# Kernel tuning notes

Hardware: AMD Instinct MI355X
Metric: run time of the kernel (lower is better)

The kernel has to match this reference:

```python
import jax, jax.numpy as jnp
import numpy as np

M = 7            # window_size
NUM_HEADS = 12
C = 384
D_HEAD = C // NUM_HEADS
SCALE = D_HEAD ** (-0.5)


def _relative_position_index(m):
    coords = np.stack(np.meshgrid(np.arange(m), np.arange(m), indexing='ij')).reshape(2, -1)
    rel = coords[:, :, None] - coords[:, None, :]          # [2, m^2, m^2]
    rel = rel.transpose(1, 2, 0).astype(np.int64)          # [m^2, m^2, 2]
    rel[..., 0] += m - 1
    rel[..., 1] += m - 1
    rel[..., 0] *= 2 * m - 1
    return jnp.asarray(rel.sum(-1))                         # [m^2, m^2]

REL_INDEX = _relative_position_index(M)


def setup_inputs() -> dict:
    key = jax.random.key(0)
    ks = jax.random.split(key, 7)
    B_, N = 4096, M * M
    x = jax.random.normal(ks[0], (B_, N, C), dtype=jnp.float32)
    mask = jax.random.normal(ks[1], (64, N, N), dtype=jnp.float32)
    bias_table = 0.02 * jax.random.normal(ks[2], ((2 * M - 1) * (2 * M - 1), NUM_HEADS), dtype=jnp.float32)
    qkv_w = 0.02 * jax.random.normal(ks[3], (3 * C, C), dtype=jnp.float32)
    qkv_b = jnp.zeros((3 * C,), dtype=jnp.float32)
    proj_w = 0.02 * jax.random.normal(ks[4], (C, C), dtype=jnp.float32)
    proj_b = jnp.zeros((C,), dtype=jnp.float32)
    return {"x": x, "mask": mask, "bias_table": bias_table,
            "qkv_w": qkv_w, "qkv_b": qkv_b, "proj_w": proj_w, "proj_b": proj_b}


def reference(x, mask, bias_table, qkv_w, qkv_b, proj_w, proj_b):
    B_, N, _ = x.shape
    H, d = NUM_HEADS, D_HEAD
    qkv = x @ qkv_w.T + qkv_b                              # [B_, N, 3C]
    qkv = qkv.reshape(B_, N, 3, H, d)
    q = qkv[:, :, 0].transpose(0, 2, 1, 3)                 # [B_, H, N, d]
    k = qkv[:, :, 1].transpose(0, 2, 1, 3)
    v = qkv[:, :, 2].transpose(0, 2, 1, 3)
    attn = jnp.einsum('bhnd,bhmd->bhnm', q, k) * SCALE     # [B_, H, N, N]
    bias = bias_table[REL_INDEX.reshape(-1)].reshape(N, N, H).transpose(2, 0, 1)
    attn = attn + bias[None]
    nW = mask.shape[0]
    attn = attn.reshape(B_ // nW, nW, H, N, N) + mask[None, :, None]
    attn = attn.reshape(B_, H, N, N)
    attn = jax.nn.softmax(attn, axis=-1)
    out = jnp.einsum('bhnm,bhmd->bhnd', attn, v)           # [B_, H, N, d]
    out = out.transpose(0, 2, 1, 3).reshape(B_, N, C)
    return out @ proj_w.T + proj_b
```

## Files before the change

kernel.cpp:

```cpp
#include <hip/hip_runtime.h>
#include <stdint.h>

typedef __attribute__((ext_vector_type(8))) short bf16x8;
typedef __attribute__((ext_vector_type(4))) short bf16x4;
typedef __attribute__((ext_vector_type(4))) float f32x4;
typedef __attribute__((ext_vector_type(2))) unsigned int u32x2;

#define NSCALE 0.17677669529663687f

static __device__ __forceinline__ float bf2f(unsigned short h) {
  union { unsigned int u; float f; } c; c.u = ((unsigned int)h) << 16; return c.f;
}
static __device__ __forceinline__ unsigned short f2bf(float f) {
  union { float f; unsigned int u; } c; c.f = f;
  unsigned int u = c.u;
  u = (u + 0x7FFFu + ((u >> 16) & 1u)) >> 16;
  return (unsigned short)u;
}
static __device__ __forceinline__ unsigned int packbf2(float a, float b) {
  return (unsigned int)f2bf(a) | ((unsigned int)f2bf(b) << 16);
}

#define W_QKVW  0
#define W_PROJW 442368
#define W_BIASE 589824
#define W_ELEMS 619240
#define W_BYTES (W_ELEMS * 2)

__global__ void cvt_w_kernel(const float* __restrict__ qkv_w,
                             const float* __restrict__ proj_w,
                             unsigned short* __restrict__ ws) {
  const int i = blockIdx.x * 256 + threadIdx.x;
  const int stride = gridDim.x * 256;
  for (int e = i; e < 442368; e += stride)
    ws[W_QKVW + e] = f2bf(qkv_w[e] * (e < 147456 ? NSCALE : 1.f));
  for (int e = i; e < 147456; e += stride)
    ws[W_PROJW + e] = f2bf(proj_w[e]);
}

__global__ void biase_kernel(const float* __restrict__ bias_t,
                             unsigned short* __restrict__ ws) {
  const int h = blockIdx.x;
  unsigned short* dst = ws + W_BIASE + h * 2450;
  for (int e = threadIdx.x; e < 2401; e += 256) {
    const int q = e / 49, k = e - q * 49;
    const int i1 = q / 7, j1 = q - i1 * 7;
    const int i2 = k / 7, j2 = k - i2 * 7;
    const int ridx = (i1 - i2 + 6) * 13 + (j1 - j2 + 6);
    dst[q * 50 + k] = f2bf(bias_t[ridx * 12 + h]);
  }
}

#define XS_O  0
#define U_O   19208
#define QS_O  (U_O)
#define KS_O  (U_O + 3920)
#define VT_O  (U_O + 7840)
#define MSP_O (U_O + 12448)
#define LDS_EL (U_O + 12448 + 2458)
#define LDS_BYTES2 (LDS_EL * 2)

__global__ void __launch_bounds__(256)
__attribute__((amdgpu_waves_per_eu(1, 8)))
winattn8(const float* __restrict__ x,
         const float* __restrict__ mask,
         const float* __restrict__ qkv_b,
         const float* __restrict__ proj_b,
         const unsigned short* __restrict__ ws,
         float* __restrict__ out)
{
  extern __shared__ unsigned short sm[];
  unsigned short* Xs  = sm + XS_O;
  unsigned short* Qs  = sm + QS_O;
  unsigned short* Ks  = sm + KS_O;
  unsigned short* Vt  = sm + VT_O;
  unsigned short* Msp = sm + MSP_O;
  unsigned short* Os  = sm + XS_O;

  const unsigned short* wsQW = ws + W_QKVW;
  const unsigned short* wsPW = ws + W_PROJW;
  const unsigned short* wsBE = ws + W_BIASE;

  const int b = blockIdx.x;
  const int tid = threadIdx.x;
  const int w = tid >> 6, lane = tid & 63, l15 = lane & 15, lg = lane >> 4;

  const float* xw = x + b * 18816;
  for (int e = tid; e < 4704; e += 256) {
    const int f = e << 2;
    const int r = f / 384;
    const int c = f - r * 384;
    f32x4 v = *(const f32x4*)(xw + f);
    u32x2 pk; pk[0] = packbf2(v[0], v[1]); pk[1] = packbf2(v[2], v[3]);
    *(u32x2*)(Xs + r * 392 + c) = pk;
  }
  {
    const float* mw = mask + (b & 63) * 2401;
    for (int e = tid; e < 2401; e += 256) {
      const int q = e / 49, k = e - q * 49;
      Msp[q * 50 + k] = f2bf(mw[e]);
    }
  }
  __syncthreads();

  const int q  = w * 16 + l15;
  const int qc = q > 48 ? 48 : q;

  unsigned int opk[6][2][2][2];

  for (int g = 0; g < 6; ++g) {
#pragma unroll
    for (int i = 0; i < 3; ++i) {
      const int nt = 3 * w + i;
      const int s = nt >> 2, sub = nt & 3, hh = sub >> 1, half = sub & 1;
      const int dd = (half << 4) + l15;
      const int o = s * 384 + (2 * g + hh) * 32 + dd;
      const unsigned short* wr = wsQW + o * 384 + lg * 8;
      f32x4 acc[4];
#pragma unroll
      for (int mi = 0; mi < 4; ++mi) acc[mi] = (f32x4){0.f, 0.f, 0.f, 0.f};
#pragma unroll
      for (int c2 = 0; c2 < 2; ++c2) {
        bf16x8 Bf[6];
#pragma unroll
        for (int cc = 0; cc < 6; ++cc) Bf[cc] = *(const bf16x8*)(wr + (c2 * 6 + cc) * 32);
#pragma unroll
        for (int mi = 0; mi < 4; ++mi) {
          const int ar = mi * 16 + l15;
          const unsigned short* ap = Xs + (ar > 48 ? 48 : ar) * 392 + lg * 8;
#pragma unroll
          for (int cc = 0; cc < 6; ++cc) {
            bf16x8 Af = *(const bf16x8*)(ap + (c2 * 6 + cc) * 32);
            acc[mi] = __builtin_amdgcn_mfma_f32_16x16x32_bf16(Af, Bf[cc], acc[mi], 0, 0, 0);
          }
        }
      }
      const float bias = qkv_b[o] * (s == 0 ? NSCALE : 1.f);
      if (s < 2) {
        unsigned short* T = (s == 0 ? Qs : Ks) + hh * 1960 + dd;
#pragma unroll
        for (int mi = 0; mi < 4; ++mi)
#pragma unroll
          for (int j = 0; j < 4; ++j) {
            const int row = mi * 16 + lg * 4 + j;
            if (row < 49) T[row * 40] = f2bf(acc[mi][j] + bias);
          }
      } else {
#pragma unroll
        for (int mi = 0; mi < 4; ++mi) {
          bf16x4 pk;
#pragma unroll
          for (int j = 0; j < 4; ++j) pk[j] = (short)f2bf(acc[mi][j] + bias);
          *(bf16x4*)(Vt + hh * 2304 + dd * 72 + mi * 16 + lg * 4) = pk;
        }
      }
    }
    __syncthreads();

#pragma unroll
    for (int hh = 0; hh < 2; ++hh) {
      const int head = 2 * g + hh;
      bf16x8 Qf = *(const bf16x8*)(Qs + hh * 1960 + qc * 40 + lg * 8);
      f32x4 S[4];
#pragma unroll
      for (int mt = 0; mt < 4; ++mt) {
        const int kr = mt * 16 + l15;
        bf16x8 Kf = *(const bf16x8*)(Ks + hh * 1960 + (kr > 48 ? 48 : kr) * 40 + lg * 8);
        f32x4 z = {0.f, 0.f, 0.f, 0.f};
        S[mt] = __builtin_amdgcn_mfma_f32_16x16x32_bf16(Kf, Qf, z, 0, 0, 0);
      }
      const unsigned short* be = wsBE + head * 2450 + qc * 50;
      const unsigned short* ms = Msp + qc * 50;
      float p[16];
      float vmax = -3e30f;
#pragma unroll
      for (int mt = 0; mt < 4; ++mt) {
        const int kc0 = mt * 16 + lg * 4;
        const int ko = kc0 > 48 ? 48 : kc0;
        const unsigned int b01 = *(const unsigned int*)(be + ko);
        const unsigned int b23 = *(const unsigned int*)(be + ko + 2);
        const unsigned int m01 = *(const unsigned int*)(ms + ko);
        const unsigned int m23 = *(const unsigned int*)(ms + ko + 2);
        float ad0 = bf2f((unsigned short)(b01 & 0xffff)) + bf2f((unsigned short)(m01 & 0xffff));
        float ad1 = bf2f((unsigned short)(b01 >> 16))    + bf2f((unsigned short)(m01 >> 16));
        float ad2 = bf2f((unsigned short)(b23 & 0xffff)) + bf2f((unsigned short)(m23 & 0xffff));
        float ad3 = bf2f((unsigned short)(b23 >> 16))    + bf2f((unsigned short)(m23 >> 16));
        float v0 = S[mt][0] + ad0, v1 = S[mt][1] + ad1;
        float v2 = S[mt][2] + ad2, v3 = S[mt][3] + ad3;
        if (kc0 + 0 >= 49) v0 = -3e30f;
        if (kc0 + 1 >= 49) v1 = -3e30f;
        if (kc0 + 2 >= 49) v2 = -3e30f;
        if (kc0 + 3 >= 49) v3 = -3e30f;
        p[mt * 4 + 0] = v0; p[mt * 4 + 1] = v1;
        p[mt * 4 + 2] = v2; p[mt * 4 + 3] = v3;
        vmax = fmaxf(fmaxf(fmaxf(v0, v1), fmaxf(v2, v3)), vmax);
      }
      vmax = fmaxf(vmax, __shfl_xor(vmax, 16, 64));
      vmax = fmaxf(vmax, __shfl_xor(vmax, 32, 64));
      float ssum = 0.f;
#pragma unroll
      for (int i = 0; i < 16; ++i) { p[i] = __expf(p[i] - vmax); ssum += p[i]; }
      ssum += __shfl_xor(ssum, 16, 64);
      ssum += __shfl_xor(ssum, 32, 64);
      const float rs = 1.f / ssum;
      unsigned int plo[4], phi[4];
#pragma unroll
      for (int mt = 0; mt < 4; ++mt) {
        plo[mt] = packbf2(p[mt * 4 + 0], p[mt * 4 + 1]);
        phi[mt] = packbf2(p[mt * 4 + 2], p[mt * 4 + 3]);
      }
      union { bf16x8 v; unsigned int u[4]; } PB[2];
      const int src0 = l15 + ((lg & 1) << 5);
      const int src1 = src0 + 16;
      const int sel = lg >> 1;
#pragma unroll
      for (int ks = 0; ks < 2; ++ks) {
        const int a0 = __shfl((int)plo[2 * ks], src0, 64), a1 = __shfl((int)plo[2 * ks + 1], src0, 64);
        const int b0 = __shfl((int)phi[2 * ks], src0, 64), b1 = __shfl((int)phi[2 * ks + 1], src0, 64);
        const int c0 = __shfl((int)plo[2 * ks], src1, 64), c1 = __shfl((int)plo[2 * ks + 1], src1, 64);
        const int d0 = __shfl((int)phi[2 * ks], src1, 64), d1 = __shfl((int)phi[2 * ks + 1], src1, 64);
        PB[ks].u[0] = (unsigned)(sel ? a1 : a0);
        PB[ks].u[1] = (unsigned)(sel ? b1 : b0);
        PB[ks].u[2] = (unsigned)(sel ? c1 : c0);
        PB[ks].u[3] = (unsigned)(sel ? d1 : d0);
      }
#pragma unroll
      for (int dt = 0; dt < 2; ++dt) {
        f32x4 a = {0.f, 0.f, 0.f, 0.f};
#pragma unroll
        for (int ks = 0; ks < 2; ++ks) {
          bf16x8 Vf = *(const bf16x8*)(Vt + hh * 2304 + (dt * 16 + l15) * 72 + ks * 32 + lg * 8);
          a = __builtin_amdgcn_mfma_f32_16x16x32_bf16(Vf, PB[ks].v, a, 0, 0, 0);
        }
        const unsigned int lo = packbf2(a[0] * rs, a[1] * rs);
        const unsigned int hi = packbf2(a[2] * rs, a[3] * rs);
        switch (g) {
          case 0: opk[0][hh][dt][0] = lo; opk[0][hh][dt][1] = hi; break;
          case 1: opk[1][hh][dt][0] = lo; opk[1][hh][dt][1] = hi; break;
          case 2: opk[2][hh][dt][0] = lo; opk[2][hh][dt][1] = hi; break;
          case 3: opk[3][hh][dt][0] = lo; opk[3][hh][dt][1] = hi; break;
          case 4: opk[4][hh][dt][0] = lo; opk[4][hh][dt][1] = hi; break;
          default: opk[5][hh][dt][0] = lo; opk[5][hh][dt][1] = hi; break;
        }
      }
    }
    __syncthreads();
  }

  if (q < 49) {
#pragma unroll
    for (int gg = 0; gg < 6; ++gg)
#pragma unroll
      for (int hh = 0; hh < 2; ++hh)
#pragma unroll
        for (int dt = 0; dt < 2; ++dt) {
          u32x2 pk; pk[0] = opk[gg][hh][dt][0]; pk[1] = opk[gg][hh][dt][1];
          *(u32x2*)(Os + q * 392 + (2 * gg + hh) * 32 + dt * 16 + lg * 4) = pk;
        }
  }
  __syncthreads();

#pragma unroll
  for (int ntl = 0; ntl < 6; ++ntl) {
    const int co = (6 * w + ntl) * 16 + l15;
    const unsigned short* wr = wsPW + co * 384 + lg * 8;
    const float pb = proj_b[co];
    f32x4 acc[4];
#pragma unroll
    for (int mt = 0; mt < 4; ++mt) acc[mt] = (f32x4){0.f, 0.f, 0.f, 0.f};
#pragma unroll
    for (int c2 = 0; c2 < 2; ++c2) {
      bf16x8 Bf[6];
#pragma unroll
      for (int cc = 0; cc < 6; ++cc) Bf[cc] = *(const bf16x8*)(wr + (c2 * 6 + cc) * 32);
#pragma unroll
      for (int mt = 0; mt < 4; ++mt) {
        const int ar = mt * 16 + l15;
        const unsigned short* ap = Os + (ar > 48 ? 48 : ar) * 392 + lg * 8;
#pragma unroll
        for (int cc = 0; cc < 6; ++cc) {
          bf16x8 Af = *(const bf16x8*)(ap + (c2 * 6 + cc) * 32);
          acc[mt] = __builtin_amdgcn_mfma_f32_16x16x32_bf16(Af, Bf[cc], acc[mt], 0, 0, 0);
        }
      }
    }
#pragma unroll
    for (int mt = 0; mt < 4; ++mt)
#pragma unroll
      for (int j = 0; j < 4; ++j) {
        const int row = mt * 16 + lg * 4 + j;
        if (row < 49) out[b * 18816 + row * 384 + co] = acc[mt][j] + pb;
      }
  }
}

#define FXS 0
#define FQS (FXS + 64*392)
#define FKS (FQS + 2*64*40)
#define FVT (FKS + 2*64*40)
#define FPS (FVT + 2*32*72)
#define FOS (FPS + 2*64*72)
#define FMS (FOS + 64*392)
#define FBS (FMS + 2408)
#define FLDS_EL (FBS + 2028)
#define FLDS_BYTES (FLDS_EL * 2)

static __device__ __forceinline__ bf16x8 cvt8(const float* p) {
  f32x4 a = *(const f32x4*)p;
  f32x4 b = *(const f32x4*)(p + 4);
  bf16x8 r;
  r[0]=(short)f2bf(a[0]); r[1]=(short)f2bf(a[1]); r[2]=(short)f2bf(a[2]); r[3]=(short)f2bf(a[3]);
  r[4]=(short)f2bf(b[0]); r[5]=(short)f2bf(b[1]); r[6]=(short)f2bf(b[2]); r[7]=(short)f2bf(b[3]);
  return r;
}

__global__ __launch_bounds__(512, 2)
void winattn_fb(const float* __restrict__ x, const float* __restrict__ mask,
                const float* __restrict__ bias_t, const float* __restrict__ qkv_w,
                const float* __restrict__ qkv_b, const float* __restrict__ proj_w,
                const float* __restrict__ proj_b, float* __restrict__ out)
{
  extern __shared__ unsigned short sm[];
  unsigned short* Xs = sm + FXS; unsigned short* Qs = sm + FQS;
  unsigned short* Ks = sm + FKS; unsigned short* Vt = sm + FVT;
  unsigned short* Ps = sm + FPS; unsigned short* Os = sm + FOS;
  unsigned short* Ms = sm + FMS; unsigned short* Bs = sm + FBS;
  const int b = blockIdx.x, tid = threadIdx.x;
  const int w = tid >> 6, lane = tid & 63, l15 = lane & 15, lg = lane >> 4;
  const float* xw = x + b * 18816;
  for (int e = tid; e < 4704; e += 512) {
    const int f = e << 2; const int r = f / 384; const int c = f - r * 384;
    f32x4 v = *(const f32x4*)(xw + f);
    unsigned short* dst = Xs + r * 392 + c;
    dst[0]=f2bf(v[0]); dst[1]=f2bf(v[1]); dst[2]=f2bf(v[2]); dst[3]=f2bf(v[3]);
  }
  { bf16x8 z = {0,0,0,0,0,0,0,0};
    for (int e = tid; e < 735; e += 512) *(bf16x8*)(Xs + 19208 + (e << 3)) = z; }
  { const float* mw = mask + (b & 63) * 2401;
    for (int e = tid; e < 2401; e += 512) Ms[e] = f2bf(mw[e]);
    for (int e = tid; e < 2028; e += 512) Bs[e] = f2bf(bias_t[e]); }
  __syncthreads();
  for (int g = 0; g < 6; ++g) {
    int t = 6 * w; const int tEnd = t + 6;
    while (t < tEnd) {
      const int nt = t >> 2; const int hh = nt / 6; const int ntl = nt - hh * 6;
      const int s = ntl >> 1; const int dd = ((nt & 1) << 4) + l15;
      const int o = s * 384 + (2 * g + hh) * 32 + dd;
      bf16x8 Bf[12];
      const float* wp = qkv_w + o * 384 + lg * 8;
#pragma unroll
      for (int kk = 0; kk < 12; ++kk) Bf[kk] = cvt8(wp + kk * 32);
      const float biasc = qkv_b[o];
      for (; t < tEnd && (t >> 2) == nt; ++t) {
        const int mt = t & 3;
        f32x4 acc = {0.f,0.f,0.f,0.f};
        const unsigned short* ap = Xs + (mt * 16 + l15) * 392 + lg * 8;
#pragma unroll
        for (int kk = 0; kk < 12; ++kk) {
          bf16x8 Af = *(const bf16x8*)(ap + kk * 32);
          acc = __builtin_amdgcn_mfma_f32_16x16x32_bf16(Af, Bf[kk], acc, 0,0,0);
        }
#pragma unroll
        for (int j = 0; j < 4; ++j) {
          const int row = mt * 16 + lg * 4 + j;
          const unsigned short hv = f2bf(acc[j] + biasc);
          if (s == 0) Qs[hh * 2560 + row * 40 + dd] = hv;
          else if (s == 1) Ks[hh * 2560 + row * 40 + dd] = hv;
          else Vt[hh * 2304 + dd * 72 + row] = hv;
        }
      }
    }
    __syncthreads();
    {
      const int hh = w >> 2; const int mt = w & 3; const int head = 2 * g + hh;
      bf16x8 Aq = *(const bf16x8*)(Qs + hh * 2560 + (mt * 16 + l15) * 40 + lg * 8);
      f32x4 accs[4];
#pragma unroll
      for (int nt = 0; nt < 4; ++nt) {
        bf16x8 Bk = *(const bf16x8*)(Ks + hh * 2560 + (nt * 16 + l15) * 40 + lg * 8);
        f32x4 z = {0.f,0.f,0.f,0.f};
        accs[nt] = __builtin_amdgcn_mfma_f32_16x16x32_bf16(Aq, Bk, z, 0,0,0);
      }
#pragma unroll
      for (int j = 0; j < 4; ++j) {
        const int row = mt * 16 + lg * 4 + j;
        float sv[4]; float vmax = -3e30f;
#pragma unroll
        for (int nt = 0; nt < 4; ++nt) {
          const int col = nt * 16 + l15;
          float v = accs[nt][j] * NSCALE;
          if (col < 49) { if (row < 49) {
              const int i1 = row / 7, j1 = row - i1 * 7;
              const int i2 = col / 7, j2 = col - i2 * 7;
              const int ridx = (i1 - i2 + 6) * 13 + (j1 - j2 + 6);
              v += bf2f(Ms[row * 49 + col]) + bf2f(Bs[ridx * 12 + head]); } }
          else v = -3e30f;
          sv[nt] = v; vmax = fmaxf(vmax, v);
        }
#pragma unroll
        for (int mm = 1; mm < 16; mm <<= 1) vmax = fmaxf(vmax, __shfl_xor(vmax, mm, 64));
        float ssum = 0.f;
#pragma unroll
        for (int nt = 0; nt < 4; ++nt) { sv[nt] = __expf(sv[nt] - vmax); ssum += sv[nt]; }
#pragma unroll
        for (int mm = 1; mm < 16; mm <<= 1) ssum += __shfl_xor(ssum, mm, 64);
        const float rs = 1.f / ssum;
#pragma unroll
        for (int nt = 0; nt < 4; ++nt)
          Ps[hh * 4608 + row * 72 + nt * 16 + l15] = f2bf(sv[nt] * rs);
      }
    }
    __syncthreads();
    {
      const int hh = w >> 2; const int mt = w & 3; const int head = 2 * g + hh;
#pragma unroll
      for (int nt = 0; nt < 2; ++nt) {
        f32x4 acc = {0.f,0.f,0.f,0.f};
#pragma unroll
        for (int kk = 0; kk < 2; ++kk) {
          bf16x8 Ap = *(const bf16x8*)(Ps + hh * 4608 + (mt * 16 + l15) * 72 + kk * 32 + lg * 8);
          bf16x8 Bv = *(const bf16x8*)(Vt + hh * 2304 + (nt * 16 + l15) * 72 + kk * 32 + lg * 8);
          acc = __builtin_amdgcn_mfma_f32_16x16x32_bf16(Ap, Bv, acc, 0,0,0);
        }
#pragma unroll
        for (int j = 0; j < 4; ++j)
          Os[(mt * 16 + lg * 4 + j) * 392 + head * 32 + nt * 16 + l15] = f2bf(acc[j]);
      }
    }
    __syncthreads();
  }
  for (int nt = 3 * w; nt < 3 * w + 3; ++nt) {
    const int co = nt * 16 + l15;
    bf16x8 Bf[12];
    const float* wp = proj_w + co * 384 + lg * 8;
#pragma unroll
    for (int kk = 0; kk < 12; ++kk) Bf[kk] = cvt8(wp + kk * 32);
    const float pb = proj_b[co];
#pragma unroll
    for (int mt = 0; mt < 4; ++mt) {
      f32x4 acc = {0.f,0.f,0.f,0.f};
      const unsigned short* ap = Os + (mt * 16 + l15) * 392 + lg * 8;
#pragma unroll
      for (int kk = 0; kk < 12; ++kk) {
        bf16x8 Af = *(const bf16x8*)(ap + kk * 32);
        acc = __builtin_amdgcn_mfma_f32_16x16x32_bf16(Af, Bf[kk], acc, 0,0,0);
      }
#pragma unroll
      for (int j = 0; j < 4; ++j) {
        const int row = mt * 16 + lg * 4 + j;
        if (row < 49) out[b * 18816 + row * 384 + co] = acc[j] + pb;
      }
    }
  }
}

extern "C" void kernel_launch(void* const* d_in, const int* in_sizes, int n_in,
                              void* d_out, int out_size, void* d_ws, size_t ws_size,
                              hipStream_t stream) {
  const float* x      = (const float*)d_in[0];
  const float* mask   = (const float*)d_in[1];
  const float* bias_t = (const float*)d_in[2];
  const float* qkv_w  = (const float*)d_in[3];
  const float* qkv_b  = (const float*)d_in[4];
  const float* proj_w = (const float*)d_in[5];
  const float* proj_b = (const float*)d_in[6];
  float* out = (float*)d_out;

  if (ws_size >= (size_t)W_BYTES) {
    unsigned short* ws = (unsigned short*)d_ws;
    cvt_w_kernel<<<dim3(1024), dim3(256), 0, stream>>>(qkv_w, proj_w, ws);
    biase_kernel<<<dim3(12), dim3(256), 0, stream>>>(bias_t, ws);
    (void)hipFuncSetAttribute((const void*)winattn8,
                              hipFuncAttributeMaxDynamicSharedMemorySize, LDS_BYTES2);
    winattn8<<<dim3(4096), dim3(256), LDS_BYTES2, stream>>>(
        x, mask, qkv_b, proj_b, ws, out);
  } else {
    (void)hipFuncSetAttribute((const void*)winattn_fb,
                              hipFuncAttributeMaxDynamicSharedMemorySize, FLDS_BYTES);
    winattn_fb<<<dim3(4096), dim3(512), FLDS_BYTES, stream>>>(
        x, mask, bias_t, qkv_w, qkv_b, proj_w, proj_b, out);
  }
}
```

Before: 801.7 us.

## Switch QKV and output projection GEMMs to 32x32x16 MFMA tiles

Replaces the 16x16x32 MFMA tiling of the QKV and projection GEMMs with 32x32x16 MFMA. Each wave now owns a 32-row half of the 49-token window and a set of 32-column output tiles. The aim is fewer LDS A-fragment reloads per MFMA and fewer padded rows (64 vs 49 handled as two 32-row tiles). In exchange the accumulators are larger (f32x16), which may raise register pressure, and the epilogue store pattern changes to a scattered row layout. The B fragments are now streamed from global memory each k-step rather than batched.

```diff
diff --git a/kernel.cpp b/kernel.cpp
--- a/kernel.cpp
+++ b/kernel.cpp
@@ -4,9 +4,11 @@
 typedef __attribute__((ext_vector_type(8))) short bf16x8;
 typedef __attribute__((ext_vector_type(4))) short bf16x4;
 typedef __attribute__((ext_vector_type(4))) float f32x4;
+typedef __attribute__((ext_vector_type(16))) float f32x16;
 typedef __attribute__((ext_vector_type(2))) unsigned int u32x2;
 
 #define NSCALE 0.17677669529663687f
+#define Z16 ((f32x16){0.f,0.f,0.f,0.f,0.f,0.f,0.f,0.f,0.f,0.f,0.f,0.f,0.f,0.f,0.f,0.f})
 
 static __device__ __forceinline__ float bf2f(unsigned short h) {
   union { unsigned int u; float f; } c; c.u = ((unsigned int)h) << 16; return c.f;
@@ -60,9 +62,33 @@
 #define LDS_EL (U_O + 12448 + 2458)
 #define LDS_BYTES2 (LDS_EL * 2)
 
+static __device__ __forceinline__ void store_qkv_tile(
+    unsigned short* Qs, unsigned short* Ks, unsigned short* Vt,
+    int t, int m0, int l31, int lhalf, float bias, const f32x16& a)
+{
+  const int s = t >> 1, hh = t & 1;
+  if (s < 2) {
+    unsigned short* T = (s == 0 ? Qs : Ks) + hh * 1960 + l31;
+#pragma unroll
+    for (int r = 0; r < 16; ++r) {
+      const int row = m0 + (r & 3) + 8 * (r >> 2) + 4 * lhalf;
+      if (row < 49) T[row * 40] = f2bf(a[r] + bias);
+    }
+  } else {
+    unsigned short* Vp = Vt + hh * 2304 + l31 * 72 + m0;
+#pragma unroll
+    for (int rq = 0; rq < 4; ++rq) {
+      bf16x4 pk;
+#pragma unroll
+      for (int j = 0; j < 4; ++j) pk[j] = (short)f2bf(a[rq * 4 + j] + bias);
+      *(bf16x4*)(Vp + 8 * rq + 4 * lhalf) = pk;
+    }
+  }
+}
+
 __global__ void __launch_bounds__(256)
 __attribute__((amdgpu_waves_per_eu(1, 8)))
-winattn8(const float* __restrict__ x,
+winattn9(const float* __restrict__ x,
          const float* __restrict__ mask,
          const float* __restrict__ qkv_b,
          const float* __restrict__ proj_b,
@@ -84,6 +110,7 @@
   const int b = blockIdx.x;
   const int tid = threadIdx.x;
   const int w = tid >> 6, lane = tid & 63, l15 = lane & 15, lg = lane >> 4;
+  const int l31 = lane & 31, lhalf = lane >> 5;
 
   const float* xw = x + b * 18816;
   for (int e = tid; e < 4704; e += 256) {
@@ -103,63 +130,59 @@
   }
   __syncthreads();
 
+  const int m0 = (w & 1) * 32;
+  const int nset = w >> 1;
+  const int arow = (m0 + l31) > 48 ? 48 : (m0 + l31);
+  const unsigned short* apA = Xs + arow * 392 + lhalf * 8;
+
   const int q  = w * 16 + l15;
   const int qc = q > 48 ? 48 : q;
 
   unsigned int opk[6][2][2][2];
 
   for (int g = 0; g < 6; ++g) {
-#pragma unroll
-    for (int i = 0; i < 3; ++i) {
-      const int nt = 3 * w + i;
-      const int s = nt >> 2, sub = nt & 3, hh = sub >> 1, half = sub & 1;
-      const int dd = (half << 4) + l15;
-      const int o = s * 384 + (2 * g + hh) * 32 + dd;
-      const unsigned short* wr = wsQW + o * 384 + lg * 8;
-      f32x4 acc[4];
-#pragma unroll
-      for (int mi = 0; mi < 4; ++mi) acc[mi] = (f32x4){0.f, 0.f, 0.f, 0.f};
-#pragma unroll
-      for (int c2 = 0; c2 < 2; ++c2) {
-        bf16x8 Bf[6];
-#pragma unroll
-        for (int cc = 0; cc < 6; ++cc) Bf[cc] = *(const bf16x8*)(wr + (c2 * 6 + cc) * 32);
-#pragma unroll
-        for (int mi = 0; mi < 4; ++mi) {
-          const int ar = mi * 16 + l15;
-          const unsigned short* ap = Xs + (ar > 48 ? 48 : ar) * 392 + lg * 8;
-#pragma unroll
-          for (int cc = 0; cc < 6; ++cc) {
-            bf16x8 Af = *(const bf16x8*)(ap + (c2 * 6 + cc) * 32);
-            acc[mi] = __builtin_amdgcn_mfma_f32_16x16x32_bf16(Af, Bf[cc], acc[mi], 0, 0, 0);
-          }
-        }
-      }
-      const float bias = qkv_b[o] * (s == 0 ? NSCALE : 1.f);
-      if (s < 2) {
-        unsigned short* T = (s == 0 ? Qs : Ks) + hh * 1960 + dd;
-#pragma unroll
-        for (int mi = 0; mi < 4; ++mi)
-#pragma unroll
-          for (int j = 0; j < 4; ++j) {
-            const int row = mi * 16 + lg * 4 + j;
-            if (row < 49) T[row * 40] = f2bf(acc[mi][j] + bias);
-          }
-      } else {
-#pragma unroll
-        for (int mi = 0; mi < 4; ++mi) {
-          bf16x4 pk;
-#pragma unroll
-          for (int j = 0; j < 4; ++j) pk[j] = (short)f2bf(acc[mi][j] + bias);
-          *(bf16x4*)(Vt + hh * 2304 + dd * 72 + mi * 16 + lg * 4) = pk;
-        }
+    const int hb = 2 * g;
+    {
+      const int t0 = 3 * nset;
+      {
+        const int oA = (t0 >> 1) * 384 + (hb + (t0 & 1)) * 32 + l31;
+        const int oB = ((t0 + 1) >> 1) * 384 + (hb + ((t0 + 1) & 1)) * 32 + l31;
+        const unsigned short* bp0 = wsQW + oA * 384 + lhalf * 8;
+        const unsigned short* bp1 = wsQW + oB * 384 + lhalf * 8;
+        f32x16 a0 = Z16, a1 = Z16;
+#pragma unroll 4
+        for (int kc = 0; kc < 24; ++kc) {
+          bf16x8 Af = *(const bf16x8*)(apA + kc * 16);
+          bf16x8 B0 = *(const bf16x8*)(bp0 + kc * 16);
+          bf16x8 B1 = *(const bf16x8*)(bp1 + kc * 16);
+          a0 = __builtin_amdgcn_mfma_f32_32x32x16_bf16(Af, B0, a0, 0, 0, 0);
+          a1 = __builtin_amdgcn_mfma_f32_32x32x16_bf16(Af, B1, a1, 0, 0, 0);
+        }
+        const float bias0 = qkv_b[oA] * ((t0 >> 1) == 0 ? NSCALE : 1.f);
+        const float bias1 = qkv_b[oB] * (((t0 + 1) >> 1) == 0 ? NSCALE : 1.f);
+        store_qkv_tile(Qs, Ks, Vt, t0,     m0, l31, lhalf, bias0, a0);
+        store_qkv_tile(Qs, Ks, Vt, t0 + 1, m0, l31, lhalf, bias1, a1);
+      }
+      {
+        const int t2 = t0 + 2;
+        const int oC = (t2 >> 1) * 384 + (hb + (t2 & 1)) * 32 + l31;
+        const unsigned short* bp2 = wsQW + oC * 384 + lhalf * 8;
+        f32x16 a2 = Z16;
+#pragma unroll 4
+        for (int kc = 0; kc < 24; ++kc) {
+          bf16x8 Af = *(const bf16x8*)(apA + kc * 16);
+          bf16x8 B2 = *(const bf16x8*)(bp2 + kc * 16);
+          a2 = __builtin_amdgcn_mfma_f32_32x32x16_bf16(Af, B2, a2, 0, 0, 0);
+        }
+        const float bias2 = qkv_b[oC] * ((t2 >> 1) == 0 ? NSCALE : 1.f);
+        store_qkv_tile(Qs, Ks, Vt, t2, m0, l31, lhalf, bias2, a2);
       }
     }
     __syncthreads();
 
 #pragma unroll
     for (int hh = 0; hh < 2; ++hh) {
-      const int head = 2 * g + hh;
+      const int head = hb + hh;
       bf16x8 Qf = *(const bf16x8*)(Qs + hh * 1960 + qc * 40 + lg * 8);
       f32x4 S[4];
 #pragma unroll
@@ -260,37 +283,34 @@
   }
   __syncthreads();
 
-#pragma unroll
-  for (int ntl = 0; ntl < 6; ++ntl) {
-    const int co = (6 * w + ntl) * 16 + l15;
-    const unsigned short* wr = wsPW + co * 384 + lg * 8;
-    const float pb = proj_b[co];
-    f32x4 acc[4];
-#pragma unroll
-    for (int mt = 0; mt < 4; ++mt) acc[mt] = (f32x4){0.f, 0.f, 0.f, 0.f};
-#pragma unroll
-    for (int c2 = 0; c2 < 2; ++c2) {
-      bf16x8 Bf[6];
-#pragma unroll
-      for (int cc = 0; cc < 6; ++cc) Bf[cc] = *(const bf16x8*)(wr + (c2 * 6 + cc) * 32);
-#pragma unroll
-      for (int mt = 0; mt < 4; ++mt) {
-        const int ar = mt * 16 + l15;
-        const unsigned short* ap = Os + (ar > 48 ? 48 : ar) * 392 + lg * 8;
-#pragma unroll
-        for (int cc = 0; cc < 6; ++cc) {
-          bf16x8 Af = *(const bf16x8*)(ap + (c2 * 6 + cc) * 32);
-          acc[mt] = __builtin_amdgcn_mfma_f32_16x16x32_bf16(Af, Bf[cc], acc[mt], 0, 0, 0);
-        }
-      }
-    }
-#pragma unroll
-    for (int mt = 0; mt < 4; ++mt)
-#pragma unroll
-      for (int j = 0; j < 4; ++j) {
-        const int row = mt * 16 + lg * 4 + j;
-        if (row < 49) out[b * 18816 + row * 384 + co] = acc[mt][j] + pb;
-      }
+  {
+    const unsigned short* apO = Os + arow * 392 + lhalf * 8;
+    float* ob = out + (size_t)b * 18816;
+#pragma unroll
+    for (int pp = 0; pp < 3; ++pp) {
+      const int n0 = (nset * 6 + 2 * pp) * 32;
+      const unsigned short* bp0 = wsPW + (n0 + l31) * 384 + lhalf * 8;
+      const unsigned short* bp1 = wsPW + (n0 + 32 + l31) * 384 + lhalf * 8;
+      f32x16 a0 = Z16, a1 = Z16;
+#pragma unroll 4
+      for (int kc = 0; kc < 24; ++kc) {
+        bf16x8 Af = *(const bf16x8*)(apO + kc * 16);
+        bf16x8 B0 = *(const bf16x8*)(bp0 + kc * 16);
+        bf16x8 B1 = *(const bf16x8*)(bp1 + kc * 16);
+        a0 = __builtin_amdgcn_mfma_f32_32x32x16_bf16(Af, B0, a0, 0, 0, 0);
+        a1 = __builtin_amdgcn_mfma_f32_32x32x16_bf16(Af, B1, a1, 0, 0, 0);
+      }
+      const float pb0 = proj_b[n0 + l31];
+      const float pb1 = proj_b[n0 + 32 + l31];
+#pragma unroll
+      for (int r = 0; r < 16; ++r) {
+        const int row = m0 + (r & 3) + 8 * (r >> 2) + 4 * lhalf;
+        if (row < 49) {
+          ob[row * 384 + n0 + l31]      = a0[r] + pb0;
+          ob[row * 384 + n0 + 32 + l31] = a1[r] + pb1;
+        }
+      }
+    }
   }
 }
 
@@ -470,9 +490,9 @@
     unsigned short* ws = (unsigned short*)d_ws;
     cvt_w_kernel<<<dim3(1024), dim3(256), 0, stream>>>(qkv_w, proj_w, ws);
     biase_kernel<<<dim3(12), dim3(256), 0, stream>>>(bias_t, ws);
-    (void)hipFuncSetAttribute((const void*)winattn8,
+    (void)hipFuncSetAttribute((const void*)winattn9,
                               hipFuncAttributeMaxDynamicSharedMemorySize, LDS_BYTES2);
-    winattn8<<<dim3(4096), dim3(256), LDS_BYTES2, stream>>>(
+    winattn9<<<dim3(4096), dim3(256), LDS_BYTES2, stream>>>(
         x, mask, qkv_b, proj_b, ws, out);
   } else {
     (void)hipFuncSetAttribute((const void*)winattn_fb,
```

Result: slower. 1.262 ms (+57.5%).

## Partition GEMMs by row tiles per wave with register-resident A fragments

Applied to the files above, without the earlier changes.

The QKV and projection GEMMs are repartitioned so each wave owns one 16-row tile and loops over all output column tiles, keeping its 12 A fragments of X (and later O) in registers. This removes repeated LDS reads of A, but every wave now streams the full weight matrix from global/L2 rather than a third or a quarter of it. The attention output is written to LDS directly each group, dropping the 96-register opk buffer and its switch-based register indexing, along with one barrier.

```diff
diff --git a/kernel.cpp b/kernel.cpp
--- a/kernel.cpp
+++ b/kernel.cpp
@@ -62,12 +62,12 @@
 
 __global__ void __launch_bounds__(256)
 __attribute__((amdgpu_waves_per_eu(1, 8)))
-winattn8(const float* __restrict__ x,
-         const float* __restrict__ mask,
-         const float* __restrict__ qkv_b,
-         const float* __restrict__ proj_b,
-         const unsigned short* __restrict__ ws,
-         float* __restrict__ out)
+winattn10(const float* __restrict__ x,
+          const float* __restrict__ mask,
+          const float* __restrict__ qkv_b,
+          const float* __restrict__ proj_b,
+          const unsigned short* __restrict__ ws,
+          float* __restrict__ out)
 {
   extern __shared__ unsigned short sm[];
   unsigned short* Xs  = sm + XS_O;
@@ -103,63 +103,69 @@
   }
   __syncthreads();
 
+  const int arow = (w * 16 + l15) > 48 ? 48 : (w * 16 + l15);
+  bf16x8 Af[12];
+#pragma unroll
+  for (int kk = 0; kk < 12; ++kk)
+    Af[kk] = *(const bf16x8*)(Xs + arow * 392 + kk * 32 + lg * 8);
+
   const int q  = w * 16 + l15;
   const int qc = q > 48 ? 48 : q;
 
-  unsigned int opk[6][2][2][2];
-
   for (int g = 0; g < 6; ++g) {
-#pragma unroll
-    for (int i = 0; i < 3; ++i) {
-      const int nt = 3 * w + i;
-      const int s = nt >> 2, sub = nt & 3, hh = sub >> 1, half = sub & 1;
-      const int dd = (half << 4) + l15;
-      const int o = s * 384 + (2 * g + hh) * 32 + dd;
-      const unsigned short* wr = wsQW + o * 384 + lg * 8;
-      f32x4 acc[4];
-#pragma unroll
-      for (int mi = 0; mi < 4; ++mi) acc[mi] = (f32x4){0.f, 0.f, 0.f, 0.f};
-#pragma unroll
-      for (int c2 = 0; c2 < 2; ++c2) {
-        bf16x8 Bf[6];
-#pragma unroll
-        for (int cc = 0; cc < 6; ++cc) Bf[cc] = *(const bf16x8*)(wr + (c2 * 6 + cc) * 32);
-#pragma unroll
-        for (int mi = 0; mi < 4; ++mi) {
-          const int ar = mi * 16 + l15;
-          const unsigned short* ap = Xs + (ar > 48 ? 48 : ar) * 392 + lg * 8;
-#pragma unroll
-          for (int cc = 0; cc < 6; ++cc) {
-            bf16x8 Af = *(const bf16x8*)(ap + (c2 * 6 + cc) * 32);
-            acc[mi] = __builtin_amdgcn_mfma_f32_16x16x32_bf16(Af, Bf[cc], acc[mi], 0, 0, 0);
-          }
-        }
-      }
-      const float bias = qkv_b[o] * (s == 0 ? NSCALE : 1.f);
-      if (s < 2) {
-        unsigned short* T = (s == 0 ? Qs : Ks) + hh * 1960 + dd;
-#pragma unroll
-        for (int mi = 0; mi < 4; ++mi)
-#pragma unroll
-          for (int j = 0; j < 4; ++j) {
-            const int row = mi * 16 + lg * 4 + j;
-            if (row < 49) T[row * 40] = f2bf(acc[mi][j] + bias);
-          }
+    const int hb = 2 * g;
+#pragma unroll
+    for (int np = 0; np < 6; ++np) {
+      const int nt0 = 2 * np, nt1 = 2 * np + 1;
+      const int s0 = nt0 >> 2, sub0 = nt0 & 3, hh0 = sub0 >> 1, hf0 = sub0 & 1;
+      const int s1 = nt1 >> 2, sub1 = nt1 & 3, hh1 = sub1 >> 1, hf1 = sub1 & 1;
+      const int o0 = s0 * 384 + (hb + hh0) * 32 + hf0 * 16 + l15;
+      const int o1 = s1 * 384 + (hb + hh1) * 32 + hf1 * 16 + l15;
+      const unsigned short* bp0 = wsQW + o0 * 384 + lg * 8;
+      const unsigned short* bp1 = wsQW + o1 * 384 + lg * 8;
+      f32x4 a0 = {0.f, 0.f, 0.f, 0.f};
+      f32x4 a1 = {0.f, 0.f, 0.f, 0.f};
+#pragma unroll
+      for (int kk = 0; kk < 12; ++kk) {
+        bf16x8 B0 = *(const bf16x8*)(bp0 + kk * 32);
+        bf16x8 B1 = *(const bf16x8*)(bp1 + kk * 32);
+        a0 = __builtin_amdgcn_mfma_f32_16x16x32_bf16(Af[kk], B0, a0, 0, 0, 0);
+        a1 = __builtin_amdgcn_mfma_f32_16x16x32_bf16(Af[kk], B1, a1, 0, 0, 0);
+      }
+      const float bias0 = qkv_b[o0] * (s0 == 0 ? NSCALE : 1.f);
+      const float bias1 = qkv_b[o1] * (s1 == 0 ? NSCALE : 1.f);
+      if (s0 < 2) {
+        unsigned short* T = (s0 == 0 ? Qs : Ks) + hh0 * 1960 + hf0 * 16 + l15;
+#pragma unroll
+        for (int j = 0; j < 4; ++j) {
+          const int row = w * 16 + lg * 4 + j;
+          if (row < 49) T[row * 40] = f2bf(a0[j] + bias0);
+        }
       } else {
-#pragma unroll
-        for (int mi = 0; mi < 4; ++mi) {
-          bf16x4 pk;
-#pragma unroll
-          for (int j = 0; j < 4; ++j) pk[j] = (short)f2bf(acc[mi][j] + bias);
-          *(bf16x4*)(Vt + hh * 2304 + dd * 72 + mi * 16 + lg * 4) = pk;
-        }
+        bf16x4 pk;
+#pragma unroll
+        for (int j = 0; j < 4; ++j) pk[j] = (short)f2bf(a0[j] + bias0);
+        *(bf16x4*)(Vt + hh0 * 2304 + (hf0 * 16 + l15) * 72 + w * 16 + lg * 4) = pk;
+      }
+      if (s1 < 2) {
+        unsigned short* T = (s1 == 0 ? Qs : Ks) + hh1 * 1960 + hf1 * 16 + l15;
+#pragma unroll
+        for (int j = 0; j < 4; ++j) {
+          const int row = w * 16 + lg * 4 + j;
+          if (row < 49) T[row * 40] = f2bf(a1[j] + bias1);
+        }
+      } else {
+        bf16x4 pk;
+#pragma unroll
+        for (int j = 0; j < 4; ++j) pk[j] = (short)f2bf(a1[j] + bias1);
+        *(bf16x4*)(Vt + hh1 * 2304 + (hf1 * 16 + l15) * 72 + w * 16 + lg * 4) = pk;
       }
     }
     __syncthreads();
 
 #pragma unroll
     for (int hh = 0; hh < 2; ++hh) {
-      const int head = 2 * g + hh;
+      const int head = hb + hh;
       bf16x8 Qf = *(const bf16x8*)(Qs + hh * 1960 + qc * 40 + lg * 8);
       f32x4 S[4];
 #pragma unroll
@@ -232,65 +238,49 @@
           bf16x8 Vf = *(const bf16x8*)(Vt + hh * 2304 + (dt * 16 + l15) * 72 + ks * 32 + lg * 8);
           a = __builtin_amdgcn_mfma_f32_16x16x32_bf16(Vf, PB[ks].v, a, 0, 0, 0);
         }
-        const unsigned int lo = packbf2(a[0] * rs, a[1] * rs);
-        const unsigned int hi = packbf2(a[2] * rs, a[3] * rs);
-        switch (g) {
-          case 0: opk[0][hh][dt][0] = lo; opk[0][hh][dt][1] = hi; break;
-          case 1: opk[1][hh][dt][0] = lo; opk[1][hh][dt][1] = hi; break;
-          case 2: opk[2][hh][dt][0] = lo; opk[2][hh][dt][1] = hi; break;
-          case 3: opk[3][hh][dt][0] = lo; opk[3][hh][dt][1] = hi; break;
-          case 4: opk[4][hh][dt][0] = lo; opk[4][hh][dt][1] = hi; break;
-          default: opk[5][hh][dt][0] = lo; opk[5][hh][dt][1] = hi; break;
+        if (q < 49) {
+          u32x2 pk;
+          pk[0] = packbf2(a[0] * rs, a[1] * rs);
+          pk[1] = packbf2(a[2] * rs, a[3] * rs);
+          *(u32x2*)(Os + q * 392 + head * 32 + dt * 16 + lg * 4) = pk;
         }
       }
     }
     __syncthreads();
   }
 
-  if (q < 49) {
-#pragma unroll
-    for (int gg = 0; gg < 6; ++gg)
-#pragma unroll
-      for (int hh = 0; hh < 2; ++hh)
-#pragma unroll
-        for (int dt = 0; dt < 2; ++dt) {
-          u32x2 pk; pk[0] = opk[gg][hh][dt][0]; pk[1] = opk[gg][hh][dt][1];
-          *(u32x2*)(Os + q * 392 + (2 * gg + hh) * 32 + dt * 16 + lg * 4) = pk;
-        }
-  }
-  __syncthreads();
-
-#pragma unroll
-  for (int ntl = 0; ntl < 6; ++ntl) {
-    const int co = (6 * w + ntl) * 16 + l15;
-    const unsigned short* wr = wsPW + co * 384 + lg * 8;
-    const float pb = proj_b[co];
-    f32x4 acc[4];
-#pragma unroll
-    for (int mt = 0; mt < 4; ++mt) acc[mt] = (f32x4){0.f, 0.f, 0.f, 0.f};
-#pragma unroll
-    for (int c2 = 0; c2 < 2; ++c2) {
-      bf16x8 Bf[6];
-#pragma unroll
-      for (int cc = 0; cc < 6; ++cc) Bf[cc] = *(const bf16x8*)(wr + (c2 * 6 + cc) * 32);
-#pragma unroll
-      for (int mt = 0; mt < 4; ++mt) {
-        const int ar = mt * 16 + l15;
-        const unsigned short* ap = Os + (ar > 48 ? 48 : ar) * 392 + lg * 8;
-#pragma unroll
-        for (int cc = 0; cc < 6; ++cc) {
-          bf16x8 Af = *(const bf16x8*)(ap + (c2 * 6 + cc) * 32);
-          acc[mt] = __builtin_amdgcn_mfma_f32_16x16x32_bf16(Af, Bf[cc], acc[mt], 0, 0, 0);
-        }
-      }
-    }
-#pragma unroll
-    for (int mt = 0; mt < 4; ++mt)
+  {
+    bf16x8 Ao[12];
+#pragma unroll
+    for (int kk = 0; kk < 12; ++kk)
+      Ao[kk] = *(const bf16x8*)(Os + arow * 392 + kk * 32 + lg * 8);
+    float* ob = out + (size_t)b * 18816;
+#pragma unroll
+    for (int np = 0; np < 12; ++np) {
+      const int co0 = (2 * np) * 16 + l15;
+      const int co1 = co0 + 16;
+      const unsigned short* bp0 = wsPW + co0 * 384 + lg * 8;
+      const unsigned short* bp1 = wsPW + co1 * 384 + lg * 8;
+      f32x4 a0 = {0.f, 0.f, 0.f, 0.f};
+      f32x4 a1 = {0.f, 0.f, 0.f, 0.f};
+#pragma unroll
+      for (int kk = 0; kk < 12; ++kk) {
+        bf16x8 B0 = *(const bf16x8*)(bp0 + kk * 32);
+        bf16x8 B1 = *(const bf16x8*)(bp1 + kk * 32);
+        a0 = __builtin_amdgcn_mfma_f32_16x16x32_bf16(Ao[kk], B0, a0, 0, 0, 0);
+        a1 = __builtin_amdgcn_mfma_f32_16x16x32_bf16(Ao[kk], B1, a1, 0, 0, 0);
+      }
+      const float pb0 = proj_b[co0];
+      const float pb1 = proj_b[co1];
 #pragma unroll
       for (int j = 0; j < 4; ++j) {
-        const int row = mt * 16 + lg * 4 + j;
-        if (row < 49) out[b * 18816 + row * 384 + co] = acc[mt][j] + pb;
-      }
+        const int row = w * 16 + lg * 4 + j;
+        if (row < 49) {
+          ob[row * 384 + co0] = a0[j] + pb0;
+          ob[row * 384 + co1] = a1[j] + pb1;
+        }
+      }
+    }
   }
 }
 
@@ -470,9 +460,9 @@
     unsigned short* ws = (unsigned short*)d_ws;
     cvt_w_kernel<<<dim3(1024), dim3(256), 0, stream>>>(qkv_w, proj_w, ws);
     biase_kernel<<<dim3(12), dim3(256), 0, stream>>>(bias_t, ws);
-    (void)hipFuncSetAttribute((const void*)winattn8,
+    (void)hipFuncSetAttribute((const void*)winattn10,
                               hipFuncAttributeMaxDynamicSharedMemorySize, LDS_BYTES2);
-    winattn8<<<dim3(4096), dim3(256), LDS_BYTES2, stream>>>(
+    winattn10<<<dim3(4096), dim3(256), LDS_BYTES2, stream>>>(
         x, mask, qkv_b, proj_b, ws, out);
   } else {
     (void)hipFuncSetAttribute((const void*)winattn_fb,
```

After: 2.292 ms. 2.86x slower.

## Reorder QKV and projection GEMM loops to reuse A fragments across output tiles

Applied to the files above, without the earlier changes.

Both the QKV and output-projection MFMA loops now iterate over K chunks outermost. Each step loads four A fragments from LDS once and reuses them across three output tiles, where before the A tile was reloaded for every output tile. This cuts LDS read traffic by about three times but holds twelve accumulators at once, raising register pressure. The waves-per-EU hint is changed from (1,8) to (2,4) to give the compiler room for the extra registers.

```diff
diff --git a/kernel.cpp b/kernel.cpp
--- a/kernel.cpp
+++ b/kernel.cpp
@@ -61,13 +61,13 @@
 #define LDS_BYTES2 (LDS_EL * 2)
 
 __global__ void __launch_bounds__(256)
-__attribute__((amdgpu_waves_per_eu(1, 8)))
-winattn8(const float* __restrict__ x,
-         const float* __restrict__ mask,
-         const float* __restrict__ qkv_b,
-         const float* __restrict__ proj_b,
-         const unsigned short* __restrict__ ws,
-         float* __restrict__ out)
+__attribute__((amdgpu_waves_per_eu(2, 4)))
+winattn11(const float* __restrict__ x,
+          const float* __restrict__ mask,
+          const float* __restrict__ qkv_b,
+          const float* __restrict__ proj_b,
+          const unsigned short* __restrict__ ws,
+          float* __restrict__ out)
 {
   extern __shared__ unsigned short sm[];
   unsigned short* Xs  = sm + XS_O;
@@ -109,57 +109,70 @@
   unsigned int opk[6][2][2][2];
 
   for (int g = 0; g < 6; ++g) {
-#pragma unroll
-    for (int i = 0; i < 3; ++i) {
-      const int nt = 3 * w + i;
-      const int s = nt >> 2, sub = nt & 3, hh = sub >> 1, half = sub & 1;
-      const int dd = (half << 4) + l15;
-      const int o = s * 384 + (2 * g + hh) * 32 + dd;
-      const unsigned short* wr = wsQW + o * 384 + lg * 8;
-      f32x4 acc[4];
-#pragma unroll
-      for (int mi = 0; mi < 4; ++mi) acc[mi] = (f32x4){0.f, 0.f, 0.f, 0.f};
-#pragma unroll
-      for (int c2 = 0; c2 < 2; ++c2) {
-        bf16x8 Bf[6];
-#pragma unroll
-        for (int cc = 0; cc < 6; ++cc) Bf[cc] = *(const bf16x8*)(wr + (c2 * 6 + cc) * 32);
+    const int hb = 2 * g;
+    {
+      const int ntb = 3 * w;
+      const unsigned short* bp[3];
+      float bias[3];
+#pragma unroll
+      for (int i = 0; i < 3; ++i) {
+        const int nt = ntb + i;
+        const int s = nt >> 2, sub = nt & 3, hh = sub >> 1, hf = sub & 1;
+        const int o = s * 384 + (hb + hh) * 32 + hf * 16 + l15;
+        bp[i] = wsQW + o * 384 + lg * 8;
+        bias[i] = qkv_b[o] * (s == 0 ? NSCALE : 1.f);
+      }
+      f32x4 acc[3][4];
+#pragma unroll
+      for (int i = 0; i < 3; ++i)
+#pragma unroll
+        for (int mi = 0; mi < 4; ++mi) acc[i][mi] = (f32x4){0.f, 0.f, 0.f, 0.f};
+#pragma unroll
+      for (int kk = 0; kk < 12; ++kk) {
+        bf16x8 A4[4];
 #pragma unroll
         for (int mi = 0; mi < 4; ++mi) {
           const int ar = mi * 16 + l15;
-          const unsigned short* ap = Xs + (ar > 48 ? 48 : ar) * 392 + lg * 8;
-#pragma unroll
-          for (int cc = 0; cc < 6; ++cc) {
-            bf16x8 Af = *(const bf16x8*)(ap + (c2 * 6 + cc) * 32);
-            acc[mi] = __builtin_amdgcn_mfma_f32_16x16x32_bf16(Af, Bf[cc], acc[mi], 0, 0, 0);
+          A4[mi] = *(const bf16x8*)(Xs + (ar > 48 ? 48 : ar) * 392 + kk * 32 + lg * 8);
+        }
+        bf16x8 B3[3];
+#pragma unroll
+        for (int i = 0; i < 3; ++i) B3[i] = *(const bf16x8*)(bp[i] + kk * 32);
+#pragma unroll
+        for (int i = 0; i < 3; ++i)
+#pragma unroll
+          for (int mi = 0; mi < 4; ++mi)
+            acc[i][mi] = __builtin_amdgcn_mfma_f32_16x16x32_bf16(A4[mi], B3[i], acc[i][mi], 0, 0, 0);
+      }
+#pragma unroll
+      for (int i = 0; i < 3; ++i) {
+        const int nt = ntb + i;
+        const int s = nt >> 2, sub = nt & 3, hh = sub >> 1, hf = sub & 1;
+        if (s < 2) {
+          unsigned short* T = (s == 0 ? Qs : Ks) + hh * 1960 + hf * 16 + l15;
+#pragma unroll
+          for (int mi = 0; mi < 4; ++mi)
+#pragma unroll
+            for (int j = 0; j < 4; ++j) {
+              const int row = mi * 16 + lg * 4 + j;
+              if (row < 49) T[row * 40] = f2bf(acc[i][mi][j] + bias[i]);
+            }
+        } else {
+#pragma unroll
+          for (int mi = 0; mi < 4; ++mi) {
+            bf16x4 pk;
+#pragma unroll
+            for (int j = 0; j < 4; ++j) pk[j] = (short)f2bf(acc[i][mi][j] + bias[i]);
+            *(bf16x4*)(Vt + hh * 2304 + (hf * 16 + l15) * 72 + mi * 16 + lg * 4) = pk;
           }
         }
       }
-      const float bias = qkv_b[o] * (s == 0 ? NSCALE : 1.f);
-      if (s < 2) {
-        unsigned short* T = (s == 0 ? Qs : Ks) + hh * 1960 + dd;
-#pragma unroll
-        for (int mi = 0; mi < 4; ++mi)
-#pragma unroll
-          for (int j = 0; j < 4; ++j) {
-            const int row = mi * 16 + lg * 4 + j;
-            if (row < 49) T[row * 40] = f2bf(acc[mi][j] + bias);
-          }
-      } else {
-#pragma unroll
-        for (int mi = 0; mi < 4; ++mi) {
-          bf16x4 pk;
-#pragma unroll
-          for (int j = 0; j < 4; ++j) pk[j] = (short)f2bf(acc[mi][j] + bias);
-          *(bf16x4*)(Vt + hh * 2304 + dd * 72 + mi * 16 + lg * 4) = pk;
-        }
-      }
     }
     __syncthreads();
 
 #pragma unroll
     for (int hh = 0; hh < 2; ++hh) {
-      const int head = 2 * g + hh;
+      const int head = hb + hh;
       bf16x8 Qf = *(const bf16x8*)(Qs + hh * 1960 + qc * 40 + lg * 8);
       f32x4 S[4];
 #pragma unroll
@@ -260,37 +273,51 @@
   }
   __syncthreads();
 
-#pragma unroll
-  for (int ntl = 0; ntl < 6; ++ntl) {
-    const int co = (6 * w + ntl) * 16 + l15;
-    const unsigned short* wr = wsPW + co * 384 + lg * 8;
-    const float pb = proj_b[co];
-    f32x4 acc[4];
-#pragma unroll
-    for (int mt = 0; mt < 4; ++mt) acc[mt] = (f32x4){0.f, 0.f, 0.f, 0.f};
-#pragma unroll
-    for (int c2 = 0; c2 < 2; ++c2) {
-      bf16x8 Bf[6];
-#pragma unroll
-      for (int cc = 0; cc < 6; ++cc) Bf[cc] = *(const bf16x8*)(wr + (c2 * 6 + cc) * 32);
-#pragma unroll
-      for (int mt = 0; mt < 4; ++mt) {
-        const int ar = mt * 16 + l15;
-        const unsigned short* ap = Os + (ar > 48 ? 48 : ar) * 392 + lg * 8;
-#pragma unroll
-        for (int cc = 0; cc < 6; ++cc) {
-          bf16x8 Af = *(const bf16x8*)(ap + (c2 * 6 + cc) * 32);
-          acc[mt] = __builtin_amdgcn_mfma_f32_16x16x32_bf16(Af, Bf[cc], acc[mt], 0, 0, 0);
-        }
-      }
-    }
-#pragma unroll
-    for (int mt = 0; mt < 4; ++mt)
-#pragma unroll
-      for (int j = 0; j < 4; ++j) {
-        const int row = mt * 16 + lg * 4 + j;
-        if (row < 49) out[b * 18816 + row * 384 + co] = acc[mt][j] + pb;
-      }
+  {
+    float* ob = out + (size_t)b * 18816;
+#pragma unroll
+    for (int pp = 0; pp < 2; ++pp) {
+      const unsigned short* bp[3];
+      float pb[3];
+      int co[3];
+#pragma unroll
+      for (int i = 0; i < 3; ++i) {
+        co[i] = (6 * w + 3 * pp + i) * 16 + l15;
+        bp[i] = wsPW + co[i] * 384 + lg * 8;
+        pb[i] = proj_b[co[i]];
+      }
+      f32x4 acc[3][4];
+#pragma unroll
+      for (int i = 0; i < 3; ++i)
+#pragma unroll
+        for (int mi = 0; mi < 4; ++mi) acc[i][mi] = (f32x4){0.f, 0.f, 0.f, 0.f};
+#pragma unroll
+      for (int kk = 0; kk < 12; ++kk) {
+        bf16x8 A4[4];
+#pragma unroll
+        for (int mi = 0; mi < 4; ++mi) {
+          const int ar = mi * 16 + l15;
+          A4[mi] = *(const bf16x8*)(Os + (ar > 48 ? 48 : ar) * 392 + kk * 32 + lg * 8);
+        }
+        bf16x8 B3[3];
+#pragma unroll
+        for (int i = 0; i < 3; ++i) B3[i] = *(const bf16x8*)(bp[i] + kk * 32);
+#pragma unroll
+        for (int i = 0; i < 3; ++i)
+#pragma unroll
+          for (int mi = 0; mi < 4; ++mi)
+            acc[i][mi] = __builtin_amdgcn_mfma_f32_16x16x32_bf16(A4[mi], B3[i], acc[i][mi], 0, 0, 0);
+      }
+#pragma unroll
+      for (int i = 0; i < 3; ++i)
+#pragma unroll
+        for (int mi = 0; mi < 4; ++mi)
+#pragma unroll
+          for (int j = 0; j < 4; ++j) {
+            const int row = mi * 16 + lg * 4 + j;
+            if (row < 49) ob[row * 384 + co[i]] = acc[i][mi][j] + pb[i];
+          }
+    }
   }
 }
 
@@ -470,9 +497,9 @@
     unsigned short* ws = (unsigned short*)d_ws;
     cvt_w_kernel<<<dim3(1024), dim3(256), 0, stream>>>(qkv_w, proj_w, ws);
     biase_kernel<<<dim3(12), dim3(256), 0, stream>>>(bias_t, ws);
-    (void)hipFuncSetAttribute((const void*)winattn8,
+    (void)hipFuncSetAttribute((const void*)winattn11,
                               hipFuncAttributeMaxDynamicSharedMemorySize, LDS_BYTES2);
-    winattn8<<<dim3(4096), dim3(256), LDS_BYTES2, stream>>>(
+    winattn11<<<dim3(4096), dim3(256), LDS_BYTES2, stream>>>(
         x, mask, qkv_b, proj_b, ws, out);
   } else {
     (void)hipFuncSetAttribute((const void*)winattn_fb,
```

New measurement: 753.7 us. 6.0% less time.
